# Kernel tuning notes

Hardware: AMD Instinct MI355X
Metric: run time of the kernel (lower is better)

## Reference

```python
import jax, jax.numpy as jnp
import numpy as np

B, TT, TP, TO = 8, 128, 256, 512
V, D, H, L = 1024, 1024, 16, 12
FF = 4 * D
DH = D // H
EPS = 1e-5


def _pe(t, d):
    # sinusoidal PE: concat(sin(omega*t), cos(omega*t)), omega = exp(-ln(1e4)*i/(d/2))
    half = d // 2
    omega = jnp.exp(-jnp.log(10000.0) * jnp.arange(half, dtype=jnp.float32) / half)
    ang = jnp.arange(t, dtype=jnp.float32)[:, None] * omega[None, :]  # (t, d/2)
    return jnp.concatenate([jnp.sin(ang), jnp.cos(ang)], axis=-1)  # (t, d)


def _ln(x, g, b):
    mu = x.mean(axis=-1, keepdims=True)
    var = ((x - mu) ** 2).mean(axis=-1, keepdims=True)
    return (x - mu) / jnp.sqrt(var + EPS) * g + b


def _forward(text_ids, prompt_ids, output_ids, text_tab, prompt_tab, output_tab, sep,
             ln1_g, ln1_b, qkv_w, out_w, out_b, ln2_g, ln2_b,
             ff1_w, ff1_b, ff2_w, ff2_b, fc_w, fc_b):
    emb = lambda ids, tab: tab[ids] + _pe(ids.shape[1], D)[None]
    sep_tok = jnp.broadcast_to(sep, (B, 1, D))
    # join: [text, sep, prompt, sep, output]
    x = jnp.concatenate([emb(text_ids, text_tab), sep_tok,
                         emb(prompt_ids, prompt_tab), sep_tok,
                         emb(output_ids, output_tab)], axis=1)  # (B, T, D)
    T = x.shape[1]
    causal = jnp.tril(jnp.ones((T, T), dtype=bool))  # (T, T)
    scale = DH ** -0.5
    neg = -jnp.finfo(x.dtype).max
    for l in range(L):
        # attention block (prenorm residual); uniform lengths -> mask m is all ones
        h = _ln(x, ln1_g[l], ln1_b[l])
        qkv = h @ qkv_w[l]  # (B, T, 3D)
        q, k, v = jnp.split(qkv, 3, axis=-1)
        q = q.reshape(B, T, H, DH)
        k = k.reshape(B, T, H, DH)
        v = v.reshape(B, T, H, DH)
        e = jnp.einsum('bihd,bjhd->bijh', q, k) * scale
        e = jnp.where(causal[None, :, :, None], e, neg)
        a = jax.nn.softmax(e, axis=2)
        o = jnp.einsum('bijh,bjhd->bihd', a, v).reshape(B, T, D)
        x = x + o @ out_w[l] + out_b[l]
        # ffn block (prenorm residual), exact GELU as torch nn.GELU default
        h2 = _ln(x, ln2_g[l], ln2_b[l])
        ff = jax.nn.gelu(h2 @ ff1_w[l] + ff1_b[l], approximate=False) @ ff2_w[l] + ff2_b[l]
        x = x + ff
    h = x @ fc_w + fc_b  # (B, T, V)
    return h[:, -1, :]  # logits of last position, (B, V)


def setup_inputs() -> dict:
    key = jax.random.key(0)
    ks = iter(jax.random.split(key, 32))
    s = 0.02
    inp = {
        'text_ids': jax.random.randint(next(ks), (B, TT), 0, V),
        'prompt_ids': jax.random.randint(next(ks), (B, TP), 0, V),
        'output_ids': jax.random.randint(next(ks), (B, TO), 0, V),
        'text_tab': jax.random.normal(next(ks), (V, D), jnp.float32) * s,
        'prompt_tab': jax.random.normal(next(ks), (V, D), jnp.float32) * s,
        'output_tab': jax.random.normal(next(ks), (V, D), jnp.float32) * s,
        'sep': jax.random.normal(next(ks), (D,), jnp.float32),
        'ln1_g': jnp.ones((L, D), jnp.float32),
        'ln1_b': jnp.zeros((L, D), jnp.float32),
        'qkv_w': jax.random.normal(next(ks), (L, D, 3 * D), jnp.float32) * s,
        'out_w': jax.random.normal(next(ks), (L, D, D), jnp.float32) * s,
        'out_b': jnp.zeros((L, D), jnp.float32),
        'ln2_g': jnp.ones((L, D), jnp.float32),
        'ln2_b': jnp.zeros((L, D), jnp.float32),
        'ff1_w': jax.random.normal(next(ks), (L, D, FF), jnp.float32) * s,
        'ff1_b': jnp.zeros((L, FF), jnp.float32),
        'ff2_w': jax.random.normal(next(ks), (L, FF, D), jnp.float32) * s,
        'ff2_b': jnp.zeros((L, D), jnp.float32),
        'fc_w': jax.random.normal(next(ks), (D, V), jnp.float32) * s,
        'fc_b': jnp.zeros((V,), jnp.float32),
    }
    return inp


def reference(text_ids, prompt_ids, output_ids, text_tab, prompt_tab, output_tab, sep,
              ln1_g, ln1_b, qkv_w, out_w, out_b, ln2_g, ln2_b,
              ff1_w, ff1_b, ff2_w, ff2_b, fc_w, fc_b):
    return _forward(text_ids, prompt_ids, output_ids, text_tab, prompt_tab, output_tab, sep,
                    ln1_g, ln1_b, qkv_w, out_w, out_b, ln2_g, ln2_b,
                    ff1_w, ff1_b, ff2_w, ff2_b, fc_w, fc_b)
```

## Files before the change

### kernel.cpp

```cpp
#include <hip/hip_runtime.h>
#include <hip/hip_bf16.h>
#include <math.h>

#define Bn 8
#define Tn 898
#define Dn 1024
#define Hn 16
#define DHn 64
#define Ln 12
#define FFn 4096
#define Vn 1024
#define BT (Bn*Tn)

typedef short bf16x8 __attribute__((ext_vector_type(8)));
typedef float f32x4 __attribute__((ext_vector_type(4)));

__device__ __forceinline__ ushort f2bf(float f) {
    union { float f; unsigned u; } c; c.f = f;
    unsigned r = c.u + 0x7fffu + ((c.u >> 16) & 1u);
    return (ushort)(r >> 16);
}

__device__ __forceinline__ void glds16(const void* g, void* l) {
    __builtin_amdgcn_global_load_lds(
        (const __attribute__((address_space(1))) unsigned int*)g,
        (__attribute__((address_space(3))) unsigned int*)l, 16, 0, 0);
}

#define BARRIER() __builtin_amdgcn_s_barrier()
#define VMCNT0() asm volatile("s_waitcnt vmcnt(0)" ::: "memory")

__global__ __launch_bounds__(256) void transpose_cast_kernel(
    const float* __restrict__ in, ushort* __restrict__ out,
    int K, int N, size_t in_ls, size_t out_ls)
{
    __shared__ ushort t[64][68];
    const float* inp = in + (size_t)blockIdx.z * in_ls;
    ushort* outp = out + (size_t)blockIdx.z * out_ls;
    int n0 = blockIdx.x * 64, k0 = blockIdx.y * 64;
    int tx = threadIdx.x & 63, ty = threadIdx.x >> 6;
    #pragma unroll
    for (int p = 0; p < 16; p++) {
        int kl = p * 4 + ty;
        t[tx][kl] = f2bf(inp[(size_t)(k0 + kl) * N + n0 + tx]);
    }
    __syncthreads();
    int tx4 = threadIdx.x & 15, ty4 = threadIdx.x >> 4;
    #pragma unroll
    for (int p = 0; p < 4; p++) {
        int nl = p * 16 + ty4;
        ushort4 v;
        v.x = t[nl][4*tx4]; v.y = t[nl][4*tx4+1]; v.z = t[nl][4*tx4+2]; v.w = t[nl][4*tx4+3];
        *(ushort4*)&outp[(size_t)(n0 + nl) * K + k0 + 4*tx4] = v;
    }
}

__global__ __launch_bounds__(256) void embed_kernel(
    const int* __restrict__ tids, const int* __restrict__ pids, const int* __restrict__ oids,
    const float* __restrict__ ttab, const float* __restrict__ ptab, const float* __restrict__ otab,
    const float* __restrict__ sep, float* __restrict__ x)
{
    int bp = blockIdx.x;
    int b = bp / Tn, pos = bp - b * Tn;
    int d0 = threadIdx.x * 4;
    float4 r;
    if (pos == 128 || pos == 385) {
        r = *(const float4*)(sep + d0);
    } else {
        int t; int id; const float* tab;
        if (pos < 128)      { t = pos;       id = tids[b*128 + t]; tab = ttab; }
        else if (pos < 385) { t = pos - 129; id = pids[b*256 + t]; tab = ptab; }
        else                { t = pos - 386; id = oids[b*512 + t]; tab = otab; }
        float4 e = *(const float4*)(tab + (size_t)id * Dn + d0);
        float pe[4];
        #pragma unroll
        for (int i = 0; i < 4; i++) {
            int d = d0 + i;
            int ii = d & 511;
            float omega = expf(-9.210340371976184f * (float)ii * (1.0f/512.0f));
            float ang = (float)t * omega;
            pe[i] = (d < 512) ? sinf(ang) : cosf(ang);
        }
        r.x = e.x + pe[0]; r.y = e.y + pe[1]; r.z = e.z + pe[2]; r.w = e.w + pe[3];
    }
    *(float4*)(x + (size_t)bp * Dn + d0) = r;
}

__global__ __launch_bounds__(256) void ln_kernel(
    const float* __restrict__ x, const float* __restrict__ g, const float* __restrict__ bt,
    ushort* __restrict__ out)
{
    int row = blockIdx.x * 4 + (threadIdx.x >> 6);
    int lane = threadIdx.x & 63;
    const float4* xr = (const float4*)(x + (size_t)row * Dn);
    float4 v[4];
    float s = 0.f;
    #pragma unroll
    for (int i = 0; i < 4; i++) {
        v[i] = xr[lane + 64 * i];
        s += v[i].x + v[i].y + v[i].z + v[i].w;
    }
    #pragma unroll
    for (int o = 32; o; o >>= 1) s += __shfl_xor(s, o);
    float mu = s * (1.0f / Dn);
    float s2 = 0.f;
    #pragma unroll
    for (int i = 0; i < 4; i++) {
        v[i].x -= mu; v[i].y -= mu; v[i].z -= mu; v[i].w -= mu;
        s2 += v[i].x*v[i].x + v[i].y*v[i].y + v[i].z*v[i].z + v[i].w*v[i].w;
    }
    #pragma unroll
    for (int o = 32; o; o >>= 1) s2 += __shfl_xor(s2, o);
    float rstd = rsqrtf(s2 * (1.0f / Dn) + 1e-5f);
    ushort4* orow = (ushort4*)(out + (size_t)row * Dn);
    #pragma unroll
    for (int i = 0; i < 4; i++) {
        float4 gg = ((const float4*)g)[lane + 64 * i];
        float4 bb = ((const float4*)bt)[lane + 64 * i];
        ushort4 o4;
        o4.x = f2bf(v[i].x * rstd * gg.x + bb.x);
        o4.y = f2bf(v[i].y * rstd * gg.y + bb.y);
        o4.z = f2bf(v[i].z * rstd * gg.z + bb.z);
        o4.w = f2bf(v[i].w * rstd * gg.w + bb.w);
        orow[lane + 64 * i] = o4;
    }
}

template<int BM, int BN, int MODE>
__global__ __launch_bounds__(256, 4) void gemmk(
    const ushort* __restrict__ A, const ushort* __restrict__ Bw,
    const float* __restrict__ bias, const float* __restrict__ resid,
    void* __restrict__ Cout, int M, int N, int K, int nx, int S)
{
    constexpr int MI = BM / 32, NI = BN / 32;
    constexpr int UA = BM / 64, UB = BN / 64;
    __shared__ ushort sA[2][BM * 32];
    __shared__ ushort sB[2][BN * 32];

    int tid = threadIdx.x, lane = tid & 63, wv = tid >> 6;
    int wm = wv >> 1, wn = wv & 1;
    int l16 = lane & 15, lhi = lane >> 4;

    int nb = gridDim.x, bid = blockIdx.x;
    int qq = nb >> 3, rr8 = nb & 7;
    int xcd = bid & 7, idx = bid >> 3;
    int wg = (xcd < rr8 ? xcd * (qq + 1) : rr8 * (qq + 1) + (xcd - rr8) * qq) + idx;

    int nmt = (M + BM - 1) / BM;
    int fullb = nmt / S, per = S * nx;
    int mt, ntt;
    if (wg < fullb * per) {
        int band = wg / per, r2 = wg - band * per;
        ntt = r2 / S; mt = band * S + (r2 - ntt * S);
    } else {
        int r2 = wg - fullb * per, bh = nmt - fullb * S;
        ntt = r2 / bh; mt = fullb * S + (r2 - ntt * bh);
    }
    int m0 = mt * BM, n0 = ntt * BN;

    f32x4 acc[MI][NI];
    #pragma unroll
    for (int i = 0; i < MI; i++)
        #pragma unroll
        for (int j = 0; j < NI; j++) acc[i][j] = (f32x4){0.f, 0.f, 0.f, 0.f};

    const size_t K2 = (size_t)K * 2;
    int srow = lane >> 2;
    int schk = ((lane & 3) ^ ((lane >> 3) & 3)) * 16;
    const char* Ap[UA];
    const char* Bp[UB];
    #pragma unroll
    for (int i = 0; i < UA; i++)
        Ap[i] = (const char*)A + (size_t)(m0 + (wv + 4 * i) * 16 + srow) * K2 + schk;
    #pragma unroll
    for (int i = 0; i < UB; i++)
        Bp[i] = (const char*)Bw + (size_t)(n0 + (wv + 4 * i) * 16 + srow) * K2 + schk;

    auto stage = [&](int buf) {
        #pragma unroll
        for (int i = 0; i < UA; i++) {
            glds16(Ap[i], (char*)sA[buf] + (wv + 4 * i) * 1024);
            Ap[i] += 64;
        }
        #pragma unroll
        for (int i = 0; i < UB; i++) {
            glds16(Bp[i], (char*)sB[buf] + (wv + 4 * i) * 1024);
            Bp[i] += 64;
        }
    };

    const int sc = (lhi ^ ((l16 >> 1) & 3)) * 8;
    auto compute = [&](int buf) {
        bf16x8 af[MI], bf[NI];
        #pragma unroll
        for (int mi = 0; mi < MI; mi++)
            af[mi] = *(const bf16x8*)&sA[buf][(wm * (16 * MI) + mi * 16 + l16) * 32 + sc];
        #pragma unroll
        for (int ni = 0; ni < NI; ni++)
            bf[ni] = *(const bf16x8*)&sB[buf][(wn * (16 * NI) + ni * 16 + l16) * 32 + sc];
        #pragma unroll
        for (int mi = 0; mi < MI; mi++)
            #pragma unroll
            for (int ni = 0; ni < NI; ni++)
                acc[mi][ni] = __builtin_amdgcn_mfma_f32_16x16x32_bf16(af[mi], bf[ni], acc[mi][ni], 0, 0, 0);
    };

    int ntile = K >> 5;
    stage(0);
    VMCNT0();
    BARRIER();
    int cur = 0;
    for (int t = 0; t < ntile; ++t) {
        if (t + 1 < ntile) stage(cur ^ 1);
        compute(cur);
        VMCNT0();
        BARRIER();
        cur ^= 1;
    }

    #pragma unroll
    for (int mi = 0; mi < MI; mi++) {
        int rl = wm * (16 * MI) + mi * 16 + lhi * 4;
        #pragma unroll
        for (int ni = 0; ni < NI; ni++) {
            int gcol = n0 + wn * (16 * NI) + ni * 16 + l16;
            float bs = (MODE == 0) ? 0.0f : bias[gcol];
            #pragma unroll
            for (int j = 0; j < 4; j++) {
                int grow = m0 + rl + j;
                if (grow >= M) continue;
                float v = acc[mi][ni][j] + bs;
                if (MODE == 1) {
                    float rv = resid[(size_t)grow * N + gcol];
                    ((float*)Cout)[(size_t)grow * N + gcol] = rv + v;
                } else if (MODE == 2) {
                    float u = v * (1.5957691216f + 0.0713548163f * v * v);
                    float g = v / (1.0f + __expf(-u));
                    ((ushort*)Cout)[(size_t)grow * N + gcol] = f2bf(g);
                } else {
                    ((ushort*)Cout)[(size_t)grow * N + gcol] = f2bf(v);
                }
            }
        }
    }
}

__global__ __launch_bounds__(256) void attn_kernel(
    const ushort* __restrict__ qkv, ushort* __restrict__ out)
{
    __shared__ ushort Ksm[64 * 72];
    __shared__ ushort Vsm[64 * 72];
    __shared__ ushort Psm[4][16 * 72];
    int qt = blockIdx.x, b = blockIdx.y, h = blockIdx.z;
    int tid = threadIdx.x, lane = tid & 63, wave = tid >> 6;
    int l16 = lane & 15, lhi = lane >> 4;

    int qrow = qt*64 + wave*16 + l16;
    bf16x8 qf0 = {}, qf1 = {};
    if (qrow < Tn) {
        const ushort* qp = qkv + (size_t)(b*Tn + qrow) * 3072 + h*64 + lhi*8;
        qf0 = *(const bf16x8*)qp;
        qf1 = *(const bf16x8*)(qp + 32);
    }

    f32x4 o[4];
    #pragma unroll
    for (int i = 0; i < 4; i++) o[i] = (f32x4){0.f,0.f,0.f,0.f};
    float mrun[4] = {-1e30f,-1e30f,-1e30f,-1e30f};
    float sume[4] = {0.f,0.f,0.f,0.f};

    int kr = tid >> 2, cc = (tid & 3) * 16;
    const ushort* kvbase = qkv + (size_t)(b*Tn) * 3072 + h*64 + cc;
    int qg = qt*64 + wave*16 + lhi*4;

    for (int jt = 0; jt <= qt; jt++) {
        int kvr = jt*64 + kr;
        uint4 k0 = make_uint4(0,0,0,0), k1 = k0, v0 = k0, v1 = k0;
        if (kvr < Tn) {
            const ushort* p = kvbase + (size_t)kvr * 3072;
            k0 = *(const uint4*)(p + 1024);
            k1 = *(const uint4*)(p + 1024 + 8);
            v0 = *(const uint4*)(p + 2048);
            v1 = *(const uint4*)(p + 2048 + 8);
        }
        __syncthreads();
        *(uint4*)&Ksm[kr * 72 + cc] = k0;
        *(uint4*)&Ksm[kr * 72 + cc + 8] = k1;
        {
            ushort vv[16];
            *(uint4*)&vv[0] = v0; *(uint4*)&vv[8] = v1;
            #pragma unroll
            for (int i = 0; i < 16; i++) Vsm[(cc + i) * 72 + kr] = vv[i];
        }
        __syncthreads();

        f32x4 s[4];
        #pragma unroll
        for (int ni = 0; ni < 4; ni++) {
            s[ni] = (f32x4){0.f,0.f,0.f,0.f};
            bf16x8 kf0 = *(const bf16x8*)&Ksm[(ni*16 + l16) * 72 + lhi*8];
            bf16x8 kf1 = *(const bf16x8*)&Ksm[(ni*16 + l16) * 72 + lhi*8 + 32];
            s[ni] = __builtin_amdgcn_mfma_f32_16x16x32_bf16(qf0, kf0, s[ni], 0, 0, 0);
            s[ni] = __builtin_amdgcn_mfma_f32_16x16x32_bf16(qf1, kf1, s[ni], 0, 0, 0);
        }

        float pv[4][4];
        #pragma unroll
        for (int j = 0; j < 4; j++) {
            int qgj = qg + j;
            float mx = -1e30f;
            #pragma unroll
            for (int ni = 0; ni < 4; ni++) {
                int kvg = jt*64 + ni*16 + l16;
                float e = (kvg <= qgj && kvg < Tn) ? s[ni][j] * 0.125f : -1e30f;
                pv[ni][j] = e;
                mx = fmaxf(mx, e);
            }
            #pragma unroll
            for (int m = 1; m < 16; m <<= 1) mx = fmaxf(mx, __shfl_xor(mx, m));
            float mnew = fmaxf(mrun[j], mx);
            float fac = expf(mrun[j] - mnew);
            mrun[j] = mnew;
            float rs = 0.f;
            #pragma unroll
            for (int ni = 0; ni < 4; ni++) { pv[ni][j] = expf(pv[ni][j] - mnew); rs += pv[ni][j]; }
            #pragma unroll
            for (int m = 1; m < 16; m <<= 1) rs += __shfl_xor(rs, m);
            sume[j] = sume[j] * fac + rs;
            #pragma unroll
            for (int di = 0; di < 4; di++) o[di][j] *= fac;
        }

        #pragma unroll
        for (int j = 0; j < 4; j++)
            #pragma unroll
            for (int ni = 0; ni < 4; ni++)
                Psm[wave][(lhi*4 + j) * 72 + ni*16 + l16] = f2bf(pv[ni][j]);
        __syncthreads();

        bf16x8 pf0 = *(const bf16x8*)&Psm[wave][l16 * 72 + lhi*8];
        bf16x8 pf1 = *(const bf16x8*)&Psm[wave][l16 * 72 + lhi*8 + 32];
        #pragma unroll
        for (int di = 0; di < 4; di++) {
            bf16x8 vf0 = *(const bf16x8*)&Vsm[(di*16 + l16) * 72 + lhi*8];
            bf16x8 vf1 = *(const bf16x8*)&Vsm[(di*16 + l16) * 72 + lhi*8 + 32];
            o[di] = __builtin_amdgcn_mfma_f32_16x16x32_bf16(pf0, vf0, o[di], 0, 0, 0);
            o[di] = __builtin_amdgcn_mfma_f32_16x16x32_bf16(pf1, vf1, o[di], 0, 0, 0);
        }
    }

    #pragma unroll
    for (int j = 0; j < 4; j++) {
        int qgj = qg + j;
        if (qgj >= Tn) continue;
        float inv = 1.0f / sume[j];
        #pragma unroll
        for (int di = 0; di < 4; di++)
            out[(size_t)(b*Tn + qgj) * Dn + h*64 + di*16 + l16] = f2bf(o[di][j] * inv);
    }
}

__global__ __launch_bounds__(256) void fc_kernel(
    const float* __restrict__ x, const float* __restrict__ w,
    const float* __restrict__ bias, float* __restrict__ out)
{
    __shared__ float xs[Dn];
    int b = blockIdx.y;
    int v = blockIdx.x * 256 + threadIdx.x;
    float4 t = ((const float4*)(x + (size_t)(b*Tn + Tn - 1) * Dn))[threadIdx.x];
    ((float4*)xs)[threadIdx.x] = t;
    __syncthreads();
    float acc = bias[v];
    for (int d = 0; d < Dn; d++)
        acc = fmaf(xs[d], w[(size_t)d * Vn + v], acc);
    out[(size_t)b * Vn + v] = acc;
}

extern "C" void kernel_launch(void* const* d_in, const int* in_sizes, int n_in,
                              void* d_out, int out_size, void* d_ws, size_t ws_size,
                              hipStream_t stream)
{
    const int*   text_ids  = (const int*)d_in[0];
    const int*   prompt_ids= (const int*)d_in[1];
    const int*   output_ids= (const int*)d_in[2];
    const float* text_tab  = (const float*)d_in[3];
    const float* prompt_tab= (const float*)d_in[4];
    const float* output_tab= (const float*)d_in[5];
    const float* sep       = (const float*)d_in[6];
    const float* ln1_g     = (const float*)d_in[7];
    const float* ln1_b     = (const float*)d_in[8];
    const float* qkv_w     = (const float*)d_in[9];
    const float* out_w     = (const float*)d_in[10];
    const float* out_b     = (const float*)d_in[11];
    const float* ln2_g     = (const float*)d_in[12];
    const float* ln2_b     = (const float*)d_in[13];
    const float* ff1_w     = (const float*)d_in[14];
    const float* ff1_b     = (const float*)d_in[15];
    const float* ff2_w     = (const float*)d_in[16];
    const float* ff2_b     = (const float*)d_in[17];
    const float* fc_w      = (const float*)d_in[18];
    const float* fc_b      = (const float*)d_in[19];

    char* ws = (char*)d_ws;
    float*  x    = (float*)(ws);
    ushort* h    = (ushort*)(ws + 29425664);
    ushort* qkv  = (ushort*)(ws + 44630016);
    ushort* attn = (ushort*)(ws + 90243072);
    ushort* ff1o = (ushort*)(ws + 105447424);
    ushort* wT   = (ushort*)(ws + 166264832);

    const size_t L_STRIDE = 12582912;
    const size_t OFF_QKV = 0, OFF_OUT = 3145728, OFF_FF1 = 4194304, OFF_FF2 = 8388608;
    const size_t upfront_need = 166264832ULL + 2ULL * L_STRIDE * Ln;
    const bool upfront = ws_size >= upfront_need;

    if (upfront) {
        transpose_cast_kernel<<<dim3(48,16,Ln), 256, 0, stream>>>(qkv_w, wT + OFF_QKV, Dn, 3*Dn, (size_t)Dn*3*Dn, L_STRIDE);
        transpose_cast_kernel<<<dim3(16,16,Ln), 256, 0, stream>>>(out_w, wT + OFF_OUT, Dn, Dn,   (size_t)Dn*Dn,   L_STRIDE);
        transpose_cast_kernel<<<dim3(64,16,Ln), 256, 0, stream>>>(ff1_w, wT + OFF_FF1, Dn, FFn,  (size_t)Dn*FFn,  L_STRIDE);
        transpose_cast_kernel<<<dim3(16,64,Ln), 256, 0, stream>>>(ff2_w, wT + OFF_FF2, FFn, Dn,  (size_t)FFn*Dn,  L_STRIDE);
    }

    embed_kernel<<<BT, 256, 0, stream>>>(text_ids, prompt_ids, output_ids,
                                         text_tab, prompt_tab, output_tab, sep, x);

    for (int l = 0; l < Ln; l++) {
        ushort* wb = upfront ? (wT + (size_t)l * L_STRIDE) : wT;
        if (!upfront) {
            transpose_cast_kernel<<<dim3(48,16,1), 256, 0, stream>>>(qkv_w + (size_t)l*Dn*3*Dn, wb + OFF_QKV, Dn, 3*Dn, 0, 0);
            transpose_cast_kernel<<<dim3(16,16,1), 256, 0, stream>>>(out_w + (size_t)l*Dn*Dn,   wb + OFF_OUT, Dn, Dn,   0, 0);
            transpose_cast_kernel<<<dim3(64,16,1), 256, 0, stream>>>(ff1_w + (size_t)l*Dn*FFn,  wb + OFF_FF1, Dn, FFn,  0, 0);
            transpose_cast_kernel<<<dim3(16,64,1), 256, 0, stream>>>(ff2_w + (size_t)l*FFn*Dn,  wb + OFF_FF2, FFn, Dn,  0, 0);
        }
        ln_kernel<<<BT/4, 256, 0, stream>>>(x, ln1_g + l*Dn, ln1_b + l*Dn, h);
        gemmk<128,128,0><<<57*24, 256, 0, stream>>>(
            h, wb + OFF_QKV, nullptr, nullptr, qkv, BT, 3*Dn, Dn, 24, 8);
        attn_kernel<<<dim3(15, Bn, Hn), 256, 0, stream>>>(qkv, attn);
        gemmk<64,128,1><<<113*8, 256, 0, stream>>>(
            attn, wb + OFF_OUT, out_b + l*Dn, x, x, BT, Dn, Dn, 8, 4);
        ln_kernel<<<BT/4, 256, 0, stream>>>(x, ln2_g + l*Dn, ln2_b + l*Dn, h);
        gemmk<128,128,2><<<57*32, 256, 0, stream>>>(
            h, wb + OFF_FF1, ff1_b + l*FFn, nullptr, ff1o, BT, FFn, Dn, 32, 8);
        gemmk<64,128,1><<<113*8, 256, 0, stream>>>(
            ff1o, wb + OFF_FF2, ff2_b + l*Dn, x, x, BT, Dn, FFn, 8, 4);
    }

    fc_kernel<<<dim3(Vn/256, Bn), 256, 0, stream>>>(x, fc_w, fc_b, (float*)d_out);
}
```

Before: 4.933 ms.

## Add 256x256 tile GEMM with 512 threads for QKV and FF1 projections

Adds a new gemm256 kernel using 256x256 output tiles, 8 waves, a 64-wide K step and a combined XOR-swizzled LDS buffer for A and B, and uses it for the QKV and FF1 GEMMs. Larger tiles raise arithmetic intensity and cut global and LDS traffic per FLOP, and the block-rasterization logic is factored into a helper. The FF2 GEMM's band parameter also changes from 4 to 6. The trade-off is fewer blocks (348 and 464 against 256 CUs), which worsens wave quantization and tail effects, and higher register and LDS pressure.

```diff
diff --git a/kernel.cpp b/kernel.cpp
--- a/kernel.cpp
+++ b/kernel.cpp
@@ -126,29 +126,13 @@
     }
 }
 
-template<int BM, int BN, int MODE>
-__global__ __launch_bounds__(256, 4) void gemmk(
-    const ushort* __restrict__ A, const ushort* __restrict__ Bw,
-    const float* __restrict__ bias, const float* __restrict__ resid,
-    void* __restrict__ Cout, int M, int N, int K, int nx, int S)
-{
-    constexpr int MI = BM / 32, NI = BN / 32;
-    constexpr int UA = BM / 64, UB = BN / 64;
-    __shared__ ushort sA[2][BM * 32];
-    __shared__ ushort sB[2][BN * 32];
-
-    int tid = threadIdx.x, lane = tid & 63, wv = tid >> 6;
-    int wm = wv >> 1, wn = wv & 1;
-    int l16 = lane & 15, lhi = lane >> 4;
-
-    int nb = gridDim.x, bid = blockIdx.x;
+__device__ __forceinline__ void raster(int nb, int bid, int nx, int S, int nmt,
+                                       int& mt, int& ntt)
+{
     int qq = nb >> 3, rr8 = nb & 7;
     int xcd = bid & 7, idx = bid >> 3;
     int wg = (xcd < rr8 ? xcd * (qq + 1) : rr8 * (qq + 1) + (xcd - rr8) * qq) + idx;
-
-    int nmt = (M + BM - 1) / BM;
     int fullb = nmt / S, per = S * nx;
-    int mt, ntt;
     if (wg < fullb * per) {
         int band = wg / per, r2 = wg - band * per;
         ntt = r2 / S; mt = band * S + (r2 - ntt * S);
@@ -156,6 +140,25 @@
         int r2 = wg - fullb * per, bh = nmt - fullb * S;
         ntt = r2 / bh; mt = fullb * S + (r2 - ntt * bh);
     }
+}
+
+template<int BM, int BN, int MODE>
+__global__ __launch_bounds__(256, 4) void gemmk(
+    const ushort* __restrict__ A, const ushort* __restrict__ Bw,
+    const float* __restrict__ bias, const float* __restrict__ resid,
+    void* __restrict__ Cout, int M, int N, int K, int nx, int S)
+{
+    constexpr int MI = BM / 32, NI = BN / 32;
+    constexpr int UA = BM / 64, UB = BN / 64;
+    __shared__ ushort sA[2][BM * 32];
+    __shared__ ushort sB[2][BN * 32];
+
+    int tid = threadIdx.x, lane = tid & 63, wv = tid >> 6;
+    int wm = wv >> 1, wn = wv & 1;
+    int l16 = lane & 15, lhi = lane >> 4;
+
+    int mt, ntt;
+    raster(gridDim.x, blockIdx.x, nx, S, (M + BM - 1) / BM, mt, ntt);
     int m0 = mt * BM, n0 = ntt * BN;
 
     f32x4 acc[MI][NI];
@@ -234,6 +237,106 @@
                     float rv = resid[(size_t)grow * N + gcol];
                     ((float*)Cout)[(size_t)grow * N + gcol] = rv + v;
                 } else if (MODE == 2) {
+                    float u = v * (1.5957691216f + 0.0713548163f * v * v);
+                    float g = v / (1.0f + __expf(-u));
+                    ((ushort*)Cout)[(size_t)grow * N + gcol] = f2bf(g);
+                } else {
+                    ((ushort*)Cout)[(size_t)grow * N + gcol] = f2bf(v);
+                }
+            }
+        }
+    }
+}
+
+template<int MODE>
+__global__ __launch_bounds__(512, 2) void gemm256(
+    const ushort* __restrict__ A, const ushort* __restrict__ Bw,
+    const float* __restrict__ bias, void* __restrict__ Cout,
+    int M, int N, int K, int nx, int S)
+{
+    __shared__ ushort sAB[2][512 * 64];
+
+    int tid = threadIdx.x, lane = tid & 63, wv = tid >> 6;
+    int wm = wv >> 2, wn = wv & 3;
+    int l16 = lane & 15, lhi = lane >> 4;
+
+    int mt, ntt;
+    raster(gridDim.x, blockIdx.x, nx, S, (M + 255) >> 8, mt, ntt);
+    int m0 = mt * 256, n0 = ntt * 256;
+
+    f32x4 acc[8][4];
+    #pragma unroll
+    for (int i = 0; i < 8; i++)
+        #pragma unroll
+        for (int j = 0; j < 4; j++) acc[i][j] = (f32x4){0.f, 0.f, 0.f, 0.f};
+
+    const size_t K2 = (size_t)K * 2;
+    int srow = lane >> 3;
+    int schk = ((lane & 7) ^ srow) * 16;
+    const char* Pp[8];
+    #pragma unroll
+    for (int i = 0; i < 8; i++) {
+        int u = wv + 8 * i;
+        int grow = (u < 32) ? (m0 + u * 8 + srow) : 0;
+        const char* base = (const char*)A;
+        if (u >= 32) { grow = n0 + (u - 32) * 8 + srow; base = (const char*)Bw; }
+        Pp[i] = base + (size_t)grow * K2 + schk;
+    }
+
+    auto stage = [&](int buf) {
+        #pragma unroll
+        for (int i = 0; i < 8; i++) {
+            glds16(Pp[i], (char*)sAB[buf] + (wv + 8 * i) * 1024);
+            Pp[i] += 128;
+        }
+    };
+
+    auto compute = [&](int buf) {
+        const ushort* Sb = sAB[buf];
+        #pragma unroll
+        for (int ks = 0; ks < 2; ks++) {
+            const int sc = (((ks << 2) | lhi) ^ (l16 & 7)) * 8;
+            bf16x8 af[8], bf[4];
+            #pragma unroll
+            for (int mi = 0; mi < 8; mi++)
+                af[mi] = *(const bf16x8*)&Sb[(wm * 128 + mi * 16 + l16) * 64 + sc];
+            #pragma unroll
+            for (int ni = 0; ni < 4; ni++)
+                bf[ni] = *(const bf16x8*)&Sb[(256 + wn * 64 + ni * 16 + l16) * 64 + sc];
+            #pragma unroll
+            for (int mi = 0; mi < 8; mi++)
+                #pragma unroll
+                for (int ni = 0; ni < 4; ni++)
+                    acc[mi][ni] = __builtin_amdgcn_mfma_f32_16x16x32_bf16(af[mi], bf[ni], acc[mi][ni], 0, 0, 0);
+        }
+    };
+
+    int ntile = K >> 6;
+    stage(0);
+    VMCNT0();
+    BARRIER();
+    int cur = 0;
+    for (int t = 0; t < ntile; ++t) {
+        if (t + 1 < ntile) stage(cur ^ 1);
+        compute(cur);
+        VMCNT0();
+        BARRIER();
+        cur ^= 1;
+    }
+
+    #pragma unroll
+    for (int mi = 0; mi < 8; mi++) {
+        int rl = wm * 128 + mi * 16 + lhi * 4;
+        #pragma unroll
+        for (int ni = 0; ni < 4; ni++) {
+            int gcol = n0 + wn * 64 + ni * 16 + l16;
+            float bs = (MODE == 0) ? 0.0f : bias[gcol];
+            #pragma unroll
+            for (int j = 0; j < 4; j++) {
+                int grow = m0 + rl + j;
+                if (grow >= M) continue;
+                float v = acc[mi][ni][j] + bs;
+                if (MODE == 2) {
                     float u = v * (1.5957691216f + 0.0713548163f * v * v);
                     float g = v / (1.0f + __expf(-u));
                     ((ushort*)Cout)[(size_t)grow * N + gcol] = f2bf(g);
@@ -433,16 +536,16 @@
             transpose_cast_kernel<<<dim3(16,64,1), 256, 0, stream>>>(ff2_w + (size_t)l*FFn*Dn,  wb + OFF_FF2, FFn, Dn,  0, 0);
         }
         ln_kernel<<<BT/4, 256, 0, stream>>>(x, ln1_g + l*Dn, ln1_b + l*Dn, h);
-        gemmk<128,128,0><<<57*24, 256, 0, stream>>>(
-            h, wb + OFF_QKV, nullptr, nullptr, qkv, BT, 3*Dn, Dn, 24, 8);
+        gemm256<0><<<29*12, 512, 0, stream>>>(
+            h, wb + OFF_QKV, nullptr, qkv, BT, 3*Dn, Dn, 12, 4);
         attn_kernel<<<dim3(15, Bn, Hn), 256, 0, stream>>>(qkv, attn);
         gemmk<64,128,1><<<113*8, 256, 0, stream>>>(
             attn, wb + OFF_OUT, out_b + l*Dn, x, x, BT, Dn, Dn, 8, 4);
         ln_kernel<<<BT/4, 256, 0, stream>>>(x, ln2_g + l*Dn, ln2_b + l*Dn, h);
-        gemmk<128,128,2><<<57*32, 256, 0, stream>>>(
-            h, wb + OFF_FF1, ff1_b + l*FFn, nullptr, ff1o, BT, FFn, Dn, 32, 8);
+        gemm256<2><<<29*16, 512, 0, stream>>>(
+            h, wb + OFF_FF1, ff1_b + l*FFn, ff1o, BT, FFn, Dn, 16, 4);
         gemmk<64,128,1><<<113*8, 256, 0, stream>>>(
-            ff1o, wb + OFF_FF2, ff2_b + l*Dn, x, x, BT, Dn, FFn, 8, 4);
+            ff1o, wb + OFF_FF2, ff2_b + l*Dn, x, x, BT, Dn, FFn, 8, 6);
     }
 
     fc_kernel<<<dim3(Vn/256, Bn), 256, 0, stream>>>(x, fc_w, fc_b, (float*)d_out);
```

Result: slower. 5.190 ms (+5.2%).

## Split FF2 GEMM along K into two partial launches plus combine kernel

Applied to the files above, without the earlier changes.

The FF2 projection (K=4096) is split into two GEMM launches, each covering half of K and writing fp32 partial sums to new workspace buffers. A new combine kernel then adds both partials, the bias and the residual into x. The launches run back to back on the same stream, so they do not execute concurrently. This shortens each launch's K loop but adds two full fp32 activation writes, the reads of those buffers and an extra kernel launch per layer, and it raises the workspace needed for upfront weight transposition.

```diff
diff --git a/kernel.cpp b/kernel.cpp
--- a/kernel.cpp
+++ b/kernel.cpp
@@ -126,29 +126,35 @@
     }
 }
 
-template<int BM, int BN, int MODE>
-__global__ __launch_bounds__(256, 4) void gemmk(
-    const ushort* __restrict__ A, const ushort* __restrict__ Bw,
-    const float* __restrict__ bias, const float* __restrict__ resid,
-    void* __restrict__ Cout, int M, int N, int K, int nx, int S)
-{
-    constexpr int MI = BM / 32, NI = BN / 32;
-    constexpr int UA = BM / 64, UB = BN / 64;
-    __shared__ ushort sA[2][BM * 32];
-    __shared__ ushort sB[2][BN * 32];
-
-    int tid = threadIdx.x, lane = tid & 63, wv = tid >> 6;
-    int wm = wv >> 1, wn = wv & 1;
-    int l16 = lane & 15, lhi = lane >> 4;
-
-    int nb = gridDim.x, bid = blockIdx.x;
+__global__ __launch_bounds__(256) void combine_kernel(
+    float* __restrict__ x, const float* __restrict__ p0, const float* __restrict__ p1,
+    const float* __restrict__ bias)
+{
+    int row = blockIdx.x * 4 + (threadIdx.x >> 6);
+    int lane = threadIdx.x & 63;
+    float4* xr = (float4*)(x + (size_t)row * Dn);
+    const float4* a0 = (const float4*)(p0 + (size_t)row * Dn);
+    const float4* a1 = (const float4*)(p1 + (size_t)row * Dn);
+    const float4* bb = (const float4*)bias;
+    #pragma unroll
+    for (int i = 0; i < 4; i++) {
+        int c = lane + 64 * i;
+        float4 v = xr[c], q0 = a0[c], q1 = a1[c], b4 = bb[c];
+        v.x += q0.x + q1.x + b4.x;
+        v.y += q0.y + q1.y + b4.y;
+        v.z += q0.z + q1.z + b4.z;
+        v.w += q0.w + q1.w + b4.w;
+        xr[c] = v;
+    }
+}
+
+__device__ __forceinline__ void raster(int nb, int bid, int nx, int S, int nmt,
+                                       int& mt, int& ntt)
+{
     int qq = nb >> 3, rr8 = nb & 7;
     int xcd = bid & 7, idx = bid >> 3;
     int wg = (xcd < rr8 ? xcd * (qq + 1) : rr8 * (qq + 1) + (xcd - rr8) * qq) + idx;
-
-    int nmt = (M + BM - 1) / BM;
     int fullb = nmt / S, per = S * nx;
-    int mt, ntt;
     if (wg < fullb * per) {
         int band = wg / per, r2 = wg - band * per;
         ntt = r2 / S; mt = band * S + (r2 - ntt * S);
@@ -156,6 +162,25 @@
         int r2 = wg - fullb * per, bh = nmt - fullb * S;
         ntt = r2 / bh; mt = fullb * S + (r2 - ntt * bh);
     }
+}
+
+template<int BM, int BN, int MODE>
+__global__ __launch_bounds__(256, 4) void gemmk(
+    const ushort* __restrict__ A, const ushort* __restrict__ Bw,
+    const float* __restrict__ bias, const float* __restrict__ resid,
+    void* __restrict__ Cout, int M, int N, int K, int Kld, int nx, int S)
+{
+    constexpr int MI = BM / 32, NI = BN / 32;
+    constexpr int UA = BM / 64, UB = BN / 64;
+    __shared__ ushort sA[2][BM * 32];
+    __shared__ ushort sB[2][BN * 32];
+
+    int tid = threadIdx.x, lane = tid & 63, wv = tid >> 6;
+    int wm = wv >> 1, wn = wv & 1;
+    int l16 = lane & 15, lhi = lane >> 4;
+
+    int mt, ntt;
+    raster(gridDim.x, blockIdx.x, nx, S, (M + BM - 1) / BM, mt, ntt);
     int m0 = mt * BM, n0 = ntt * BN;
 
     f32x4 acc[MI][NI];
@@ -164,7 +189,7 @@
         #pragma unroll
         for (int j = 0; j < NI; j++) acc[i][j] = (f32x4){0.f, 0.f, 0.f, 0.f};
 
-    const size_t K2 = (size_t)K * 2;
+    const size_t K2 = (size_t)Kld * 2;
     int srow = lane >> 2;
     int schk = ((lane & 3) ^ ((lane >> 3) & 3)) * 16;
     const char* Ap[UA];
@@ -224,7 +249,7 @@
         #pragma unroll
         for (int ni = 0; ni < NI; ni++) {
             int gcol = n0 + wn * (16 * NI) + ni * 16 + l16;
-            float bs = (MODE == 0) ? 0.0f : bias[gcol];
+            float bs = (MODE == 1 || MODE == 2) ? bias[gcol] : 0.0f;
             #pragma unroll
             for (int j = 0; j < 4; j++) {
                 int grow = m0 + rl + j;
@@ -237,6 +262,8 @@
                     float u = v * (1.5957691216f + 0.0713548163f * v * v);
                     float g = v / (1.0f + __expf(-u));
                     ((ushort*)Cout)[(size_t)grow * N + gcol] = f2bf(g);
+                } else if (MODE == 3) {
+                    ((float*)Cout)[(size_t)grow * N + gcol] = v;
                 } else {
                     ((ushort*)Cout)[(size_t)grow * N + gcol] = f2bf(v);
                 }
@@ -407,11 +434,13 @@
     ushort* qkv  = (ushort*)(ws + 44630016);
     ushort* attn = (ushort*)(ws + 90243072);
     ushort* ff1o = (ushort*)(ws + 105447424);
-    ushort* wT   = (ushort*)(ws + 166264832);
+    float*  p0   = (float*)(ws + 166264832);
+    float*  p1   = (float*)(ws + 195690496);
+    ushort* wT   = (ushort*)(ws + 225116160);
 
     const size_t L_STRIDE = 12582912;
     const size_t OFF_QKV = 0, OFF_OUT = 3145728, OFF_FF1 = 4194304, OFF_FF2 = 8388608;
-    const size_t upfront_need = 166264832ULL + 2ULL * L_STRIDE * Ln;
+    const size_t upfront_need = 225116160ULL + 2ULL * L_STRIDE * Ln;
     const bool upfront = ws_size >= upfront_need;
 
     if (upfront) {
@@ -434,15 +463,18 @@
         }
         ln_kernel<<<BT/4, 256, 0, stream>>>(x, ln1_g + l*Dn, ln1_b + l*Dn, h);
         gemmk<128,128,0><<<57*24, 256, 0, stream>>>(
-            h, wb + OFF_QKV, nullptr, nullptr, qkv, BT, 3*Dn, Dn, 24, 8);
+            h, wb + OFF_QKV, nullptr, nullptr, qkv, BT, 3*Dn, Dn, Dn, 24, 8);
         attn_kernel<<<dim3(15, Bn, Hn), 256, 0, stream>>>(qkv, attn);
         gemmk<64,128,1><<<113*8, 256, 0, stream>>>(
-            attn, wb + OFF_OUT, out_b + l*Dn, x, x, BT, Dn, Dn, 8, 4);
+            attn, wb + OFF_OUT, out_b + l*Dn, x, x, BT, Dn, Dn, Dn, 8, 4);
         ln_kernel<<<BT/4, 256, 0, stream>>>(x, ln2_g + l*Dn, ln2_b + l*Dn, h);
         gemmk<128,128,2><<<57*32, 256, 0, stream>>>(
-            h, wb + OFF_FF1, ff1_b + l*FFn, nullptr, ff1o, BT, FFn, Dn, 32, 8);
-        gemmk<64,128,1><<<113*8, 256, 0, stream>>>(
-            ff1o, wb + OFF_FF2, ff2_b + l*Dn, x, x, BT, Dn, FFn, 8, 4);
+            h, wb + OFF_FF1, ff1_b + l*FFn, nullptr, ff1o, BT, FFn, Dn, Dn, 32, 8);
+        gemmk<64,128,3><<<113*8, 256, 0, stream>>>(
+            ff1o, wb + OFF_FF2, nullptr, nullptr, p0, BT, Dn, FFn/2, FFn, 8, 4);
+        gemmk<64,128,3><<<113*8, 256, 0, stream>>>(
+            ff1o + FFn/2, wb + OFF_FF2 + FFn/2, nullptr, nullptr, p1, BT, Dn, FFn/2, FFn, 8, 4);
+        combine_kernel<<<BT/4, 256, 0, stream>>>(x, p0, p1, ff2_b + l*Dn);
     }
 
     fc_kernel<<<dim3(Vn/256, Bn), 256, 0, stream>>>(x, fc_w, fc_b, (float*)d_out);
```

New measurement: 5.141 ms. 1.04x slower.
